# Kernel optimization log

Hardware: AMD Instinct MI355X
Metric: run time of the kernel (lower is better)

Reference implementation:

```python
import jax, jax.numpy as jnp
import numpy as np

B, T, A = 1024, 64, 6
STOCH, DETER, HIDDEN, EMBED = 30, 200, 200, 1024
RSSM_STD = 0.1


def setup_inputs() -> dict:
    key = jax.random.key(0)
    ks = jax.random.split(key, 20)
    r = lambda k, shape, scale=0.05: (jax.random.normal(k, shape, jnp.float32) * scale)
    inp = {
        'embed': jax.random.normal(ks[0], (B, T, EMBED), jnp.float32),
        'action': jax.random.normal(ks[1], (B, T, A), jnp.float32),
        'noise_prior': jax.random.normal(ks[2], (B, T, STOCH), jnp.float32),
        'noise_post': jax.random.normal(ks[3], (B, T, STOCH), jnp.float32),
        # fc_input: Linear(stoch+A -> hidden)
        'Wi': r(ks[4], (HIDDEN, STOCH + A)), 'bi': jnp.zeros((HIDDEN,), jnp.float32),
        # GRUCell(hidden -> deter)
        'W_ih': r(ks[5], (3 * DETER, HIDDEN)), 'W_hh': r(ks[6], (3 * DETER, DETER)),
        'b_ih': jnp.zeros((3 * DETER,), jnp.float32), 'b_hh': jnp.zeros((3 * DETER,), jnp.float32),
        # fc_prior: Linear(deter->hidden), ELU, Linear(hidden->2*stoch)
        'Wp1': r(ks[7], (HIDDEN, DETER)), 'bp1': jnp.zeros((HIDDEN,), jnp.float32),
        'Wp2': r(ks[8], (2 * STOCH, HIDDEN)), 'bp2': jnp.zeros((2 * STOCH,), jnp.float32),
        # fc_post: Linear(deter+embed->hidden), ELU, Linear(hidden->2*stoch)
        'Wq1': r(ks[9], (HIDDEN, DETER + EMBED)), 'bq1': jnp.zeros((HIDDEN,), jnp.float32),
        'Wq2': r(ks[10], (2 * STOCH, HIDDEN)), 'bq2': jnp.zeros((2 * STOCH,), jnp.float32),
    }
    return inp


def _gru_cell(x, h, W_ih, W_hh, b_ih, b_hh):
    gi = x @ W_ih.T + b_ih  # (B, 3*deter)
    gh = h @ W_hh.T + b_hh
    i_r, i_z, i_n = jnp.split(gi, 3, axis=-1)
    h_r, h_z, h_n = jnp.split(gh, 3, axis=-1)
    r = jax.nn.sigmoid(i_r + h_r)
    z = jax.nn.sigmoid(i_z + h_z)
    n = jnp.tanh(i_n + r * h_n)
    return (1.0 - z) * n + z * h


def reference(embed, action, noise_prior, noise_post,
              Wi, bi, W_ih, W_hh, b_ih, b_hh,
              Wp1, bp1, Wp2, bp2, Wq1, bq1, Wq2, bq2):
    # observe(): scan over time; carry = (post_stoch, deter)
    def step(carry, inp):
        stoch, deter = carry
        a_t, e_t, np_t, nq_t = inp
        # img_step
        x = jax.nn.elu(jnp.concatenate([stoch, a_t], -1) @ Wi.T + bi)
        deter_new = _gru_cell(x, deter, W_ih, W_hh, b_ih, b_hh)
        hp = jax.nn.elu(deter_new @ Wp1.T + bp1)
        pm, ps = jnp.split(hp @ Wp2.T + bp2, 2, axis=-1)
        ps = jax.nn.softplus(ps) + RSSM_STD
        pst = np_t * ps + pm
        # posterior
        hq = jax.nn.elu(jnp.concatenate([deter_new, e_t], -1) @ Wq1.T + bq1)
        qm, qs = jnp.split(hq @ Wq2.T + bq2, 2, axis=-1)
        qs = jax.nn.softplus(qs) + RSSM_STD
        qst = nq_t * qs + qm
        out = jnp.concatenate([qm, qs, qst, deter_new, pm, ps, pst, deter_new], -1)
        return (qst, deter_new), out

    Bsz = action.shape[0]
    init = (jnp.zeros((Bsz, STOCH), action.dtype), jnp.zeros((Bsz, DETER), action.dtype))
    xs = (jnp.swapaxes(action, 0, 1), jnp.swapaxes(embed, 0, 1),
          jnp.swapaxes(noise_prior, 0, 1), jnp.swapaxes(noise_post, 0, 1))
    _, outs = jax.lax.scan(step, init, xs)  # (T, B, 2*(3*stoch+deter))
    # (B, T, 580): [post_mean, post_std, post_stoch, post_deter, prior_mean, prior_std, prior_stoch, prior_deter]
    return jnp.swapaxes(outs, 0, 1)
```

## Files before the change

### kernel.cpp

```cpp
#include <hip/hip_runtime.h>
#include <math.h>

typedef unsigned short u16;
typedef unsigned int   u32;
typedef __attribute__((ext_vector_type(8))) short short8;
typedef __attribute__((ext_vector_type(4))) float f32x4;

#define NBATCH 1024
#define NT 64
#define OC 580
#define RB 16
#define SCAN_BLOCKS (NBATCH / RB)
#define SX 232
#define SF 212

#define P_WI    0
#define P_WIH   26624
#define P_WHH   306176
#define P_WQ1   585728
#define P_WQ2   678912
#define P_EB    707584
#define P_WP1   1133568
#define P_WP2   1226752
#define P_TOTAL 1255424

__device__ __forceinline__ float elu_f(float x) { return x > 0.f ? x : __expf(x) - 1.f; }
__device__ __forceinline__ float sig_f(float x) { return __fdividef(1.f, 1.f + __expf(-x)); }
__device__ __forceinline__ float sp_f(float x)  { return x > 20.f ? x : log1pf(__expf(x)); }
__device__ __forceinline__ float tanh_f(float x) {
    float ax = fabsf(x); ax = ax > 10.f ? 10.f : ax;
    float e = __expf(2.f * ax);
    float t = __fdividef(e - 1.f, e + 1.f);
    return copysignf(t, x);
}

__device__ __forceinline__ void bar_lds() {
    __builtin_amdgcn_sched_barrier(0);
    asm volatile("s_waitcnt lgkmcnt(0)" ::: "memory");
    __builtin_amdgcn_s_barrier();
    __builtin_amdgcn_sched_barrier(0);
}

__device__ __forceinline__ u16 f2b(float f) {
    union { float f; u32 u; } v; v.f = f;
    u32 r = (v.u + 0x7fffu + ((v.u >> 16) & 1u)) >> 16;
    return (u16)r;
}

__device__ __forceinline__ short8 pack8(float4 v0, float4 v1) {
    short8 r;
    r[0] = (short)f2b(v0.x); r[1] = (short)f2b(v0.y);
    r[2] = (short)f2b(v0.z); r[3] = (short)f2b(v0.w);
    r[4] = (short)f2b(v1.x); r[5] = (short)f2b(v1.y);
    r[6] = (short)f2b(v1.z); r[7] = (short)f2b(v1.w);
    return r;
}

#define MFMA(a, b, c) __builtin_amdgcn_mfma_f32_16x16x32_bf16((a), (b), (c), 0, 0, 0)

__global__ __launch_bounds__(256) void prep_pack(
    const float* __restrict__ Wi, const float* __restrict__ W_ih,
    const float* __restrict__ W_hh, const float* __restrict__ Wq1,
    const float* __restrict__ Wq2, const float* __restrict__ Wp1,
    const float* __restrict__ Wp2, u16* __restrict__ wp)
{
    for (size_t r = (size_t)blockIdx.x * 256 + threadIdx.x; r < P_TOTAL;
         r += (size_t)gridDim.x * 256) {
        float val = 0.f;
        if (r < P_WIH) {
            int tile = r / 1024, lane = (r % 1024) / 8, el = r % 8;
            int tt = tile / 2, ks = tile % 2;
            int j = tt * 16 + (lane & 15), k = ks * 32 + (lane >> 4) * 8 + el;
            if (j < 200 && k < 36 && lane < 64) val = Wi[j * 36 + k];
        } else if (r < P_WHH) {
            size_t q = r - P_WIH;
            int tile = q / 1024, lane = (q % 1024) / 8, el = q % 8;
            int g = tile / 91, rem = tile % 91, tt = rem / 7, ks = rem % 7;
            int j = tt * 16 + (lane & 15), k = ks * 32 + (lane >> 4) * 8 + el;
            if (j < 200 && k < 200 && lane < 64) val = W_ih[(size_t)(g * 200 + j) * 200 + k];
        } else if (r < P_WQ1) {
            size_t q = r - P_WHH;
            int tile = q / 1024, lane = (q % 1024) / 8, el = q % 8;
            int g = tile / 91, rem = tile % 91, tt = rem / 7, ks = rem % 7;
            int j = tt * 16 + (lane & 15), k = ks * 32 + (lane >> 4) * 8 + el;
            if (j < 200 && k < 200 && lane < 64) val = W_hh[(size_t)(g * 200 + j) * 200 + k];
        } else if (r < P_WQ2) {
            size_t q = r - P_WQ1;
            int tile = q / 1024, lane = (q % 1024) / 8, el = q % 8;
            int tt = tile / 7, ks = tile % 7;
            int j = tt * 16 + (lane & 15), k = ks * 32 + (lane >> 4) * 8 + el;
            if (j < 200 && k < 200 && lane < 64) val = Wq1[(size_t)j * 1224 + k];
        } else if (r < P_EB) {
            size_t q = r - P_WQ2;
            int tile = q / 1024, lane = (q % 1024) / 8, el = q % 8;
            int tt = tile / 7, ks = tile % 7;
            int j = tt * 16 + (lane & 15), k = ks * 32 + (lane >> 4) * 8 + el;
            if (j < 60 && k < 200 && lane < 64) val = Wq2[(size_t)j * 200 + k];
        } else if (r < P_WP1) {
            size_t q = r - P_EB;
            int tile = q / 1024, lane = (q % 1024) / 8, el = q % 8;
            int ks = tile / 13, tt = tile % 13;
            int j = tt * 16 + (lane & 15), k = ks * 32 + (lane >> 4) * 8 + el;
            if (j < 200 && lane < 64) val = Wq1[(size_t)j * 1224 + 200 + k];
        } else if (r < P_WP2) {
            size_t q = r - P_WP1;
            int tile = q / 1024, lane = (q % 1024) / 8, el = q % 8;
            int ks = tile / 13, tt = tile % 13;
            int j = tt * 16 + (lane & 15), k = ks * 32 + (lane >> 4) * 8 + el;
            if (j < 200 && k < 200 && lane < 64) val = Wp1[(size_t)j * 200 + k];
        } else {
            size_t q = r - P_WP2;
            int tile = q / 1024, lane = (q % 1024) / 8, el = q % 8;
            int ks = tile / 4, tt = tile % 4;
            int j = tt * 16 + (lane & 15), k = ks * 32 + (lane >> 4) * 8 + el;
            if (j < 60 && k < 200 && lane < 64) val = Wp2[(size_t)j * 200 + k];
        }
        wp[r] = f2b(val);
    }
}

__global__ __launch_bounds__(512) void epre_mfma(
    const float* __restrict__ embed, const u16* __restrict__ wp,
    const float* __restrict__ bq1, float* __restrict__ out)
{
    const int tid = threadIdx.x;
    const int wv = tid >> 6, ln = tid & 63;
    const int arow = ln & 15, kgrp = ln >> 4;
    const int m0 = blockIdx.x * 256 + wv * 32;

    f32x4 acc[2][13];
    #pragma unroll
    for (int tt = 0; tt < 13; ++tt) {
        const int j = tt * 16 + arow;
        const float bv = (j < 200) ? bq1[j] : 0.f;
        acc[0][tt] = (f32x4){bv, bv, bv, bv};
        acc[1][tt] = acc[0][tt];
    }
    const float* e0 = &embed[(size_t)(m0 + arow) * 1024 + kgrp * 8];
    const float* e1 = e0 + (size_t)16 * 1024;

    for (int ks = 0; ks < 32; ++ks) {
        short8 a0, a1;
        {
            float4 v0 = *(const float4*)(e0 + ks * 32);
            float4 v1 = *(const float4*)(e0 + ks * 32 + 4);
            a0 = pack8(v0, v1);
            float4 w0 = *(const float4*)(e1 + ks * 32);
            float4 w1 = *(const float4*)(e1 + ks * 32 + 4);
            a1 = pack8(w0, w1);
        }
        const u16* bp = &wp[P_EB + (size_t)ks * 13 * 1024 + (size_t)ln * 8];
        #pragma unroll
        for (int tt = 0; tt < 13; ++tt) {
            short8 b = *(const short8*)(bp + (size_t)tt * 1024);
            acc[0][tt] = MFMA(a0, b, acc[0][tt]);
            acc[1][tt] = MFMA(a1, b, acc[1][tt]);
        }
    }
    #pragma unroll
    for (int f = 0; f < 2; ++f) {
        const size_t rbase = (size_t)(m0 + f * 16 + kgrp * 4);
        #pragma unroll
        for (int tt = 0; tt < 13; ++tt) {
            const int j = tt * 16 + arow;
            if (j < 200) {
                #pragma unroll
                for (int e = 0; e < 4; ++e)
                    out[(rbase + e) * OC + 290 + j] = acc[f][tt][e];
            }
        }
    }
}

__global__ __launch_bounds__(512, 2) void scan_mfma(
    const float* __restrict__ action, const float* __restrict__ noise_post,
    const float* __restrict__ b_ih, const float* __restrict__ b_hh,
    const float* __restrict__ bi, const float* __restrict__ bq2,
    const u16* __restrict__ wp, float* __restrict__ out)
{
    __shared__ u16   s_in0[RB][72];
    __shared__ u16   s_x[RB][SX];
    __shared__ u16   s_db[RB][SX];
    __shared__ u16   s_hq[RB][SX];
    __shared__ float s_df[RB][200];
    __shared__ float s_ep[2][RB][SF];
    __shared__ float s_r[RB][SF], s_z[RB][SF], s_inn[RB][SF], s_hnn[RB][SF];
    __shared__ float s_q[RB][64];
    __shared__ float s_bih[3][208], s_bhh[3][208], s_bi[208], s_bq2[64];

    const int tid  = threadIdx.x;
    const int wv   = tid >> 6, ln = tid & 63;
    const int arow = ln & 15, kgrp = ln >> 4;
    const int b0   = blockIdx.x * RB;
    const int ia   = tid / 6, ca = tid - (tid / 6) * 6;

    { u32* z = (u32*)s_in0; for (int i = tid; i < RB*72/2;  i += 512) z[i] = 0; }
    { u32* z = (u32*)s_x;   for (int i = tid; i < RB*SX/2;  i += 512) z[i] = 0; }
    { u32* z = (u32*)s_db;  for (int i = tid; i < RB*SX/2;  i += 512) z[i] = 0; }
    { u32* z = (u32*)s_hq;  for (int i = tid; i < RB*SX/2;  i += 512) z[i] = 0; }
    { float* z = (float*)s_ep; for (int i = tid; i < 2*RB*SF; i += 512) z[i] = 0.f; }
    { float* z = (float*)s_df; for (int i = tid; i < RB*200; i += 512) z[i] = 0.f; }
    for (int i = tid; i < 3 * 208; i += 512) {
        int g = i / 208, j = i % 208;
        s_bih[g][j] = j < 200 ? b_ih[g * 200 + j] : 0.f;
        s_bhh[g][j] = j < 200 ? b_hh[g * 200 + j] : 0.f;
    }
    for (int i = tid; i < 208; i += 512) s_bi[i] = i < 200 ? bi[i] : 0.f;
    if (tid < 64) s_bq2[tid] = tid < 60 ? bq2[tid] : 0.f;

    short8 whhP[5][7];
    #pragma unroll
    for (int q = 0; q < 5; ++q) {
        int p = wv + 8 * q; int pe = p < 39 ? p : 0;
        #pragma unroll
        for (int ks = 0; ks < 7; ++ks)
            whhP[q][ks] = *(const short8*)&wp[P_WHH + ((size_t)pe * 7 + ks) * 1024 + ln * 8];
    }
    __syncthreads();

    for (int idx = tid; idx < RB * 200; idx += 512) {
        int i = idx / 200, j = idx - i * 200;
        s_ep[0][i][j] = out[((size_t)(b0 + i) * NT + 0) * OC + 290 + j];
    }
    if (tid < 96)
        s_in0[ia][30 + ca] = f2b(action[((size_t)(b0 + ia) * NT + 0) * 6 + ca]);
    __syncthreads();

    for (int t = 0; t < NT; ++t) {
        const int p0 = t & 1, p1 = (t + 1) & 1;
        const bool pN = (t + 1 < NT);

        for (int tt = wv; tt < 13; tt += 8) {
            float bv = s_bi[tt * 16 + arow];
            f32x4 acc = {bv, bv, bv, bv};
            #pragma unroll
            for (int ks = 0; ks < 2; ++ks) {
                short8 af = *(const short8*)&s_in0[arow][ks * 32 + kgrp * 8];
                short8 wf = *(const short8*)&wp[P_WI + (size_t)(tt * 2 + ks) * 1024 + ln * 8];
                acc = MFMA(af, wf, acc);
            }
            #pragma unroll
            for (int e = 0; e < 4; ++e)
                s_x[kgrp * 4 + e][tt * 16 + arow] = f2b(elu_f(acc[e]));
        }
        bar_lds();

        {
            f32x4 gi[5], gh[5];
            #pragma unroll
            for (int q = 0; q < 5; ++q) {
                int p = wv + 8 * q; int pe = p < 39 ? p : 0;
                int g = pe / 13, tt = pe % 13;
                float b1 = s_bih[g][tt * 16 + arow];
                float b2 = s_bhh[g][tt * 16 + arow];
                gi[q] = (f32x4){b1, b1, b1, b1};
                gh[q] = (f32x4){b2, b2, b2, b2};
            }
            #pragma unroll
            for (int ks = 0; ks < 7; ++ks) {
                short8 ax = *(const short8*)&s_x[arow][ks * 32 + kgrp * 8];
                short8 ad = *(const short8*)&s_db[arow][ks * 32 + kgrp * 8];
                #pragma unroll
                for (int q = 0; q < 5; ++q) {
                    int p = wv + 8 * q; int pe = p < 39 ? p : 0;
                    short8 w1 = *(const short8*)&wp[P_WIH + ((size_t)pe * 7 + ks) * 1024 + ln * 8];
                    gi[q] = MFMA(ax, w1, gi[q]);
                    gh[q] = MFMA(ad, whhP[q][ks], gh[q]);
                }
            }
            #pragma unroll
            for (int q = 0; q < 5; ++q) {
                int p = wv + 8 * q;
                if (p < 39) {
                    int g = p / 13, tt = p % 13, j = tt * 16 + arow;
                    #pragma unroll
                    for (int e = 0; e < 4; ++e) {
                        int i = kgrp * 4 + e;
                        if (g == 0)      s_r[i][j] = sig_f(gi[q][e] + gh[q][e]);
                        else if (g == 1) s_z[i][j] = sig_f(gi[q][e] + gh[q][e]);
                        else { s_inn[i][j] = gi[q][e]; s_hnn[i][j] = gh[q][e]; }
                    }
                }
            }
        }
        bar_lds();

        {
            float epp[7];
            if (pN) {
                #pragma unroll
                for (int q = 0; q < 7; ++q) {
                    int idx = tid + q * 512;
                    if (idx < RB * 200) {
                        int i = idx / 200, j = idx - i * 200;
                        epp[q] = out[((size_t)(b0 + i) * NT + (t + 1)) * OC + 290 + j];
                    }
                }
            }
            for (int idx = tid; idx < RB * 200; idx += 512) {
                int i = idx / 200, j = idx % 200;
                float rr = s_r[i][j], zz = s_z[i][j];
                float nn = tanh_f(s_inn[i][j] + rr * s_hnn[i][j]);
                float d = (1.f - zz) * nn + zz * s_df[i][j];
                s_df[i][j] = d;
                s_db[i][j] = f2b(d);
                size_t o = ((size_t)(b0 + i) * NT + t) * OC;
                out[o + 90 + j]  = d;
                out[o + 380 + j] = d;
            }
            if (pN) {
                #pragma unroll
                for (int q = 0; q < 7; ++q) {
                    int idx = tid + q * 512;
                    if (idx < RB * 200) {
                        int i = idx / 200, j = idx - i * 200;
                        s_ep[p1][i][j] = epp[q];
                    }
                }
            }
        }
        bar_lds();

        float nz = 0.f, actp = 0.f;
        if (tid < RB * 30)
            nz = noise_post[((size_t)(b0 + tid / 30) * NT + t) * 30 + (tid % 30)];
        if (pN && tid < 96)
            actp = action[((size_t)(b0 + ia) * NT + (t + 1)) * 6 + ca];
        for (int tt = wv; tt < 13; tt += 8) {
            int j = tt * 16 + arow;
            f32x4 acc;
            #pragma unroll
            for (int e = 0; e < 4; ++e) acc[e] = s_ep[p0][kgrp * 4 + e][j];
            for (int ks = 0; ks < 7; ++ks) {
                short8 ad = *(const short8*)&s_db[arow][ks * 32 + kgrp * 8];
                short8 wf = *(const short8*)&wp[P_WQ1 + ((size_t)tt * 7 + ks) * 1024 + ln * 8];
                acc = MFMA(ad, wf, acc);
            }
            #pragma unroll
            for (int e = 0; e < 4; ++e)
                s_hq[kgrp * 4 + e][j] = f2b(elu_f(acc[e]));
        }
        bar_lds();

        if (wv < 4) {
            int tt = wv, j = tt * 16 + arow;
            float bv = s_bq2[j];
            f32x4 acc = {bv, bv, bv, bv};
            for (int ks = 0; ks < 7; ++ks) {
                short8 ah = *(const short8*)&s_hq[arow][ks * 32 + kgrp * 8];
                short8 wf = *(const short8*)&wp[P_WQ2 + ((size_t)tt * 7 + ks) * 1024 + ln * 8];
                acc = MFMA(ah, wf, acc);
            }
            #pragma unroll
            for (int e = 0; e < 4; ++e) s_q[kgrp * 4 + e][j] = acc[e];
        }
        bar_lds();

        if (tid < RB * 30) {
            int i = tid / 30, s = tid % 30;
            float qm = s_q[i][s];
            float qs = sp_f(s_q[i][30 + s]) + 0.1f;
            size_t bt = (size_t)(b0 + i) * NT + t;
            float qst = nz * qs + qm;
            size_t o = bt * OC;
            out[o + s]      = qm;
            out[o + 30 + s] = qs;
            out[o + 60 + s] = qst;
            s_in0[i][s] = f2b(qst);
        }
        if (pN && tid < 96)
            s_in0[ia][30 + ca] = f2b(actp);
        bar_lds();
    }
}

__global__ __launch_bounds__(256) void prior_mfma(
    const float* __restrict__ noise_prior, const u16* __restrict__ wp,
    const float* __restrict__ bp1, const float* __restrict__ bp2,
    float* __restrict__ out)
{
    __shared__ __align__(16) u16   s_hp[64][232];
    __shared__ __align__(16) float s_p[64][68];
    const int tid = threadIdx.x;
    const int wv = tid >> 6, ln = tid & 63;
    const int arow = ln & 15, kgrp = ln >> 4;
    const size_t bt0 = (size_t)blockIdx.x * 64;
    const int m0 = wv * 16;

    for (int idx = tid; idx < 64 * 32; idx += 256) {
        int r2 = idx >> 5, c = 200 + (idx & 31);
        s_hp[r2][c] = 0;
    }

    f32x4 acc[13];
    #pragma unroll
    for (int tt = 0; tt < 13; ++tt) {
        const int j = tt * 16 + arow;
        const float bv = (j < 200) ? bp1[j] : 0.f;
        acc[tt] = (f32x4){bv, bv, bv, bv};
    }
    for (int ks = 0; ks < 7; ++ks) {
        short8 a;
        const int k0 = ks * 32 + kgrp * 8;
        if (k0 <= 192) {
            const float* dp = &out[(bt0 + m0 + arow) * OC + 380 + k0];
            float4 v0 = *(const float4*)dp;
            float4 v1 = *(const float4*)(dp + 4);
            a = pack8(v0, v1);
        } else {
            a = (short8){0, 0, 0, 0, 0, 0, 0, 0};
        }
        const u16* bp = &wp[P_WP1 + (size_t)ks * 13 * 1024 + (size_t)ln * 8];
        #pragma unroll
        for (int tt = 0; tt < 13; ++tt)
            acc[tt] = MFMA(a, *(const short8*)(bp + (size_t)tt * 1024), acc[tt]);
    }
    #pragma unroll
    for (int tt = 0; tt < 13; ++tt)
        #pragma unroll
        for (int e = 0; e < 4; ++e)
            s_hp[m0 + kgrp * 4 + e][tt * 16 + arow] = f2b(elu_f(acc[tt][e]));
    __syncthreads();

    f32x4 acc2[4];
    #pragma unroll
    for (int tt = 0; tt < 4; ++tt) {
        const int j = tt * 16 + arow;
        const float bv = (j < 60) ? bp2[j] : 0.f;
        acc2[tt] = (f32x4){bv, bv, bv, bv};
    }
    #pragma unroll
    for (int ks = 0; ks < 7; ++ks) {
        short8 ah = *(const short8*)&s_hp[m0 + arow][ks * 32 + kgrp * 8];
        const u16* bp = &wp[P_WP2 + (size_t)ks * 4 * 1024 + (size_t)ln * 8];
        #pragma unroll
        for (int tt = 0; tt < 4; ++tt)
            acc2[tt] = MFMA(ah, *(const short8*)(bp + (size_t)tt * 1024), acc2[tt]);
    }
    #pragma unroll
    for (int tt = 0; tt < 4; ++tt)
        #pragma unroll
        for (int e = 0; e < 4; ++e)
            s_p[m0 + kgrp * 4 + e][tt * 16 + arow] = acc2[tt][e];
    __syncthreads();

    for (int idx = tid; idx < 64 * 30; idx += 256) {
        int i = idx / 30, ss = idx - i * 30;
        float pm = s_p[i][ss];
        float ps = sp_f(s_p[i][30 + ss]) + 0.1f;
        float pst = noise_prior[(bt0 + i) * 30 + ss] * ps + pm;
        size_t base = (bt0 + i) * OC;
        out[base + 290 + ss] = pm;
        out[base + 320 + ss] = ps;
        out[base + 350 + ss] = pst;
    }
}

extern "C" void kernel_launch(void* const* d_in, const int* in_sizes, int n_in,
                              void* d_out, int out_size, void* d_ws, size_t ws_size,
                              hipStream_t stream)
{
    (void)in_sizes; (void)n_in; (void)out_size; (void)ws_size;
    const float* embed       = (const float*)d_in[0];
    const float* action      = (const float*)d_in[1];
    const float* noise_prior = (const float*)d_in[2];
    const float* noise_post  = (const float*)d_in[3];
    const float* Wi   = (const float*)d_in[4];
    const float* bi   = (const float*)d_in[5];
    const float* W_ih = (const float*)d_in[6];
    const float* W_hh = (const float*)d_in[7];
    const float* b_ih = (const float*)d_in[8];
    const float* b_hh = (const float*)d_in[9];
    const float* Wp1  = (const float*)d_in[10];
    const float* bp1  = (const float*)d_in[11];
    const float* Wp2  = (const float*)d_in[12];
    const float* bp2  = (const float*)d_in[13];
    const float* Wq1  = (const float*)d_in[14];
    const float* bq1  = (const float*)d_in[15];
    const float* Wq2  = (const float*)d_in[16];
    const float* bq2  = (const float*)d_in[17];
    float* out = (float*)d_out;
    u16* wp = (u16*)d_ws;

    hipLaunchKernelGGL(prep_pack, dim3((P_TOTAL + 255) / 256), dim3(256), 0, stream,
                       Wi, W_ih, W_hh, Wq1, Wq2, Wp1, Wp2, wp);
    hipLaunchKernelGGL(epre_mfma, dim3(256), dim3(512), 0, stream,
                       embed, wp, bq1, out);
    hipLaunchKernelGGL(scan_mfma, dim3(SCAN_BLOCKS), dim3(512), 0, stream,
                       action, noise_post, b_ih, b_hh, bi, bq2, wp, out);
    hipLaunchKernelGGL(prior_mfma, dim3(NBATCH * NT / 64), dim3(256), 0, stream,
                       noise_prior, wp, bp1, bp2, out);
}
```

Before: 1.342 ms.

## Fuse GRU gate nonlinearity into MFMA epilogue and remap waves to column tiles

Each wave now owns whole column tiles across all three GRU gates, so the r/z/n gate math and the state update run in registers right after the MFMA loop. This removes the s_r/s_z/s_inn/s_hnn staging arrays and one block barrier per timestep. The register-cached W_hh fragments are dropped and reloaded from global each step, which frees registers but adds global/L2 traffic. Prefetch of the next step's encoder projection and action moves onto the three waves that own only one tile, evening out the uneven work split.

```diff
diff --git a/kernel.cpp b/kernel.cpp
--- a/kernel.cpp
+++ b/kernel.cpp
@@ -184,7 +184,6 @@
     __shared__ u16   s_hq[RB][SX];
     __shared__ float s_df[RB][200];
     __shared__ float s_ep[2][RB][SF];
-    __shared__ float s_r[RB][SF], s_z[RB][SF], s_inn[RB][SF], s_hnn[RB][SF];
     __shared__ float s_q[RB][64];
     __shared__ float s_bih[3][208], s_bhh[3][208], s_bi[208], s_bq2[64];
 
@@ -192,7 +191,6 @@
     const int wv   = tid >> 6, ln = tid & 63;
     const int arow = ln & 15, kgrp = ln >> 4;
     const int b0   = blockIdx.x * RB;
-    const int ia   = tid / 6, ca = tid - (tid / 6) * 6;
 
     { u32* z = (u32*)s_in0; for (int i = tid; i < RB*72/2;  i += 512) z[i] = 0; }
     { u32* z = (u32*)s_x;   for (int i = tid; i < RB*SX/2;  i += 512) z[i] = 0; }
@@ -207,24 +205,24 @@
     }
     for (int i = tid; i < 208; i += 512) s_bi[i] = i < 200 ? bi[i] : 0.f;
     if (tid < 64) s_bq2[tid] = tid < 60 ? bq2[tid] : 0.f;
-
-    short8 whhP[5][7];
-    #pragma unroll
-    for (int q = 0; q < 5; ++q) {
-        int p = wv + 8 * q; int pe = p < 39 ? p : 0;
-        #pragma unroll
-        for (int ks = 0; ks < 7; ++ks)
-            whhP[q][ks] = *(const short8*)&wp[P_WHH + ((size_t)pe * 7 + ks) * 1024 + ln * 8];
-    }
     __syncthreads();
 
     for (int idx = tid; idx < RB * 200; idx += 512) {
         int i = idx / 200, j = idx - i * 200;
         s_ep[0][i][j] = out[((size_t)(b0 + i) * NT + 0) * OC + 290 + j];
     }
-    if (tid < 96)
+    if (tid < 96) {
+        int ia = tid / 6, ca = tid - (tid / 6) * 6;
         s_in0[ia][30 + ca] = f2b(action[((size_t)(b0 + ia) * NT + 0) * 6 + ca]);
+    }
     __syncthreads();
+
+    const int  t0 = wv, t1 = wv + 8;
+    const bool has2 = (t1 < 13);
+    const int  j0 = t0 * 16 + arow;
+    const int  j1 = t1 * 16 + arow;
+    const bool lightw = (wv >= 5);
+    const int  ll = (wv - 5) * 64 + ln;
 
     for (int t = 0; t < NT; ++t) {
         const int p0 = t & 1, p1 = (t + 1) & 1;
@@ -246,86 +244,96 @@
         bar_lds();
 
         {
-            f32x4 gi[5], gh[5];
-            #pragma unroll
-            for (int q = 0; q < 5; ++q) {
-                int p = wv + 8 * q; int pe = p < 39 ? p : 0;
-                int g = pe / 13, tt = pe % 13;
-                float b1 = s_bih[g][tt * 16 + arow];
-                float b2 = s_bhh[g][tt * 16 + arow];
-                gi[q] = (f32x4){b1, b1, b1, b1};
-                gh[q] = (f32x4){b2, b2, b2, b2};
+            float epv[17]; float av = 0.f;
+            if (lightw && pN) {
+                #pragma unroll
+                for (int k = 0; k < 17; ++k) {
+                    int idx = ll + k * 192;
+                    if (idx < RB * 200) {
+                        int i = idx / 200, j = idx - i * 200;
+                        epv[k] = out[((size_t)(b0 + i) * NT + (t + 1)) * OC + 290 + j];
+                    }
+                }
+                if (ll < 96)
+                    av = action[((size_t)(b0 + ll / 6) * NT + (t + 1)) * 6 + (ll % 6)];
+            }
+
+            f32x4 gi0[3], gh0[3], gi1[3], gh1[3];
+            #pragma unroll
+            for (int g = 0; g < 3; ++g) {
+                float b1 = s_bih[g][j0], b2 = s_bhh[g][j0];
+                gi0[g] = (f32x4){b1, b1, b1, b1};
+                gh0[g] = (f32x4){b2, b2, b2, b2};
+                float c1 = has2 ? s_bih[g][j1] : 0.f;
+                float c2 = has2 ? s_bhh[g][j1] : 0.f;
+                gi1[g] = (f32x4){c1, c1, c1, c1};
+                gh1[g] = (f32x4){c2, c2, c2, c2};
             }
             #pragma unroll
             for (int ks = 0; ks < 7; ++ks) {
                 short8 ax = *(const short8*)&s_x[arow][ks * 32 + kgrp * 8];
                 short8 ad = *(const short8*)&s_db[arow][ks * 32 + kgrp * 8];
                 #pragma unroll
-                for (int q = 0; q < 5; ++q) {
-                    int p = wv + 8 * q; int pe = p < 39 ? p : 0;
-                    short8 w1 = *(const short8*)&wp[P_WIH + ((size_t)pe * 7 + ks) * 1024 + ln * 8];
-                    gi[q] = MFMA(ax, w1, gi[q]);
-                    gh[q] = MFMA(ad, whhP[q][ks], gh[q]);
-                }
-            }
-            #pragma unroll
-            for (int q = 0; q < 5; ++q) {
-                int p = wv + 8 * q;
-                if (p < 39) {
-                    int g = p / 13, tt = p % 13, j = tt * 16 + arow;
+                for (int g = 0; g < 3; ++g) {
+                    gi0[g] = MFMA(ax, *(const short8*)&wp[P_WIH + ((size_t)(g*13 + t0)*7 + ks)*1024 + ln*8], gi0[g]);
+                    gh0[g] = MFMA(ad, *(const short8*)&wp[P_WHH + ((size_t)(g*13 + t0)*7 + ks)*1024 + ln*8], gh0[g]);
+                }
+                if (has2) {
                     #pragma unroll
-                    for (int e = 0; e < 4; ++e) {
-                        int i = kgrp * 4 + e;
-                        if (g == 0)      s_r[i][j] = sig_f(gi[q][e] + gh[q][e]);
-                        else if (g == 1) s_z[i][j] = sig_f(gi[q][e] + gh[q][e]);
-                        else { s_inn[i][j] = gi[q][e]; s_hnn[i][j] = gh[q][e]; }
+                    for (int g = 0; g < 3; ++g) {
+                        gi1[g] = MFMA(ax, *(const short8*)&wp[P_WIH + ((size_t)(g*13 + t1)*7 + ks)*1024 + ln*8], gi1[g]);
+                        gh1[g] = MFMA(ad, *(const short8*)&wp[P_WHH + ((size_t)(g*13 + t1)*7 + ks)*1024 + ln*8], gh1[g]);
                     }
                 }
             }
-        }
-        bar_lds();
-
-        {
-            float epp[7];
-            if (pN) {
-                #pragma unroll
-                for (int q = 0; q < 7; ++q) {
-                    int idx = tid + q * 512;
+            if (j0 < 200) {
+                #pragma unroll
+                for (int e = 0; e < 4; ++e) {
+                    int i = kgrp * 4 + e;
+                    float rr = sig_f(gi0[0][e] + gh0[0][e]);
+                    float zz = sig_f(gi0[1][e] + gh0[1][e]);
+                    float nn = tanh_f(gi0[2][e] + rr * gh0[2][e]);
+                    float d = (1.f - zz) * nn + zz * s_df[i][j0];
+                    s_df[i][j0] = d;
+                    s_db[i][j0] = f2b(d);
+                    size_t o = ((size_t)(b0 + i) * NT + t) * OC;
+                    out[o + 90 + j0]  = d;
+                    out[o + 380 + j0] = d;
+                }
+            }
+            if (has2 && j1 < 200) {
+                #pragma unroll
+                for (int e = 0; e < 4; ++e) {
+                    int i = kgrp * 4 + e;
+                    float rr = sig_f(gi1[0][e] + gh1[0][e]);
+                    float zz = sig_f(gi1[1][e] + gh1[1][e]);
+                    float nn = tanh_f(gi1[2][e] + rr * gh1[2][e]);
+                    float d = (1.f - zz) * nn + zz * s_df[i][j1];
+                    s_df[i][j1] = d;
+                    s_db[i][j1] = f2b(d);
+                    size_t o = ((size_t)(b0 + i) * NT + t) * OC;
+                    out[o + 90 + j1]  = d;
+                    out[o + 380 + j1] = d;
+                }
+            }
+            if (lightw && pN) {
+                #pragma unroll
+                for (int k = 0; k < 17; ++k) {
+                    int idx = ll + k * 192;
                     if (idx < RB * 200) {
                         int i = idx / 200, j = idx - i * 200;
-                        epp[q] = out[((size_t)(b0 + i) * NT + (t + 1)) * OC + 290 + j];
+                        s_ep[p1][i][j] = epv[k];
                     }
                 }
-            }
-            for (int idx = tid; idx < RB * 200; idx += 512) {
-                int i = idx / 200, j = idx % 200;
-                float rr = s_r[i][j], zz = s_z[i][j];
-                float nn = tanh_f(s_inn[i][j] + rr * s_hnn[i][j]);
-                float d = (1.f - zz) * nn + zz * s_df[i][j];
-                s_df[i][j] = d;
-                s_db[i][j] = f2b(d);
-                size_t o = ((size_t)(b0 + i) * NT + t) * OC;
-                out[o + 90 + j]  = d;
-                out[o + 380 + j] = d;
-            }
-            if (pN) {
-                #pragma unroll
-                for (int q = 0; q < 7; ++q) {
-                    int idx = tid + q * 512;
-                    if (idx < RB * 200) {
-                        int i = idx / 200, j = idx - i * 200;
-                        s_ep[p1][i][j] = epp[q];
-                    }
-                }
+                if (ll < 96)
+                    s_in0[ll / 6][30 + (ll % 6)] = f2b(av);
             }
         }
         bar_lds();
 
-        float nz = 0.f, actp = 0.f;
+        float nz = 0.f;
         if (tid < RB * 30)
             nz = noise_post[((size_t)(b0 + tid / 30) * NT + t) * 30 + (tid % 30)];
-        if (pN && tid < 96)
-            actp = action[((size_t)(b0 + ia) * NT + (t + 1)) * 6 + ca];
         for (int tt = wv; tt < 13; tt += 8) {
             int j = tt * 16 + arow;
             f32x4 acc;
@@ -368,8 +376,6 @@
             out[o + 60 + s] = qst;
             s_in0[i][s] = f2b(qst);
         }
-        if (pN && tid < 96)
-            s_in0[ia][30 + ca] = f2b(actp);
         bar_lds();
     }
 }
```

Measured after the change: 1.712 ms. 27.6% more time.
